# Kernel optimization log

Measured on AMD Instinct MI355X. Metric: run time of the kernel, lower is better.

The kernel has to match this reference:

```python
import jax, jax.numpy as jnp
import numpy as np

NUM_INTERNAL = 4000
MAX_CHILDREN = 16
BATCH = 1024


def _build_tree():
    # Deterministic synthetic hierarchy: child counts in [2, 16].
    counts = 2 + (np.arange(NUM_INTERNAL) * 7) % 15
    row = np.repeat(np.arange(NUM_INTERNAL), counts)
    col = np.concatenate([np.arange(n) for n in counts])
    flat_index = row * MAX_CHILDREN + col          # scatter slots in padded buffer
    num_nodes = int(counts.sum()) + 1              # +1 for the root
    child_index = np.arange(1, num_nodes)          # every non-root node is a child once
    return flat_index, child_index, num_nodes


def setup_inputs() -> dict:
    flat_index, child_index, num_nodes = _build_tree()
    key = jax.random.key(0)
    scores = jax.random.normal(key, (BATCH, flat_index.shape[0]), dtype=jnp.float32)
    return {
        "scores": scores,
        "flat_index": jnp.asarray(flat_index, dtype=jnp.int32),
        "child_index": jnp.asarray(child_index, dtype=jnp.int32),
        "num_internal": NUM_INTERNAL,
        "max_num_children": MAX_CHILDREN,
        "num_nodes": num_nodes,
    }


def reference(scores, flat_index, child_index, num_internal, max_num_children, num_nodes):
    lead = scores.shape[:-1]
    neg_inf = jnp.asarray(-jnp.inf, scores.dtype)
    # Scatter scores into padded [num_internal, max_num_children] buffer (-inf padding).
    flat = jnp.full((*lead, num_internal * max_num_children), neg_inf, dtype=scores.dtype)
    flat = flat.at[..., flat_index].set(scores)
    # Per-internal-node (grouped) log-softmax over the padded child axis.
    child_log_p = jax.nn.log_softmax(
        flat.reshape(*lead, num_internal, max_num_children), axis=-1
    ).reshape(*lead, num_internal * max_num_children)
    # Gather real slots back and scatter into node-indexed output (root stays 0).
    out = jnp.zeros((*lead, num_nodes), dtype=scores.dtype)
    out = out.at[..., child_index].set(child_log_p[..., flat_index])
    return out


if __name__ == "__main__":
    inp = setup_inputs()
    y = reference(**inp)
    print(y.shape, y.dtype)
```

## Files before the change

kernel.cpp:

```cpp
#include <hip/hip_runtime.h>
#include <math.h>

#define MAXC 16
#define GPB  256
#define BLOCK 256
#define LBUF_SZ (GPB * MAXC + 32)

__global__ void build_meta_kernel(const int* __restrict__ flat_index,
                                  const int* __restrict__ p_num_internal,
                                  const int* __restrict__ p_max_children,
                                  int n_scores,
                                  int* __restrict__ offs,
                                  unsigned short* __restrict__ gid16) {
    int j = blockIdx.x * blockDim.x + threadIdx.x;
    int mc = p_max_children[0];
    if (j < n_scores) {
        int fi = flat_index[j];
        int g  = fi / mc;
        gid16[j] = (unsigned short)g;
        if (fi - g * mc == 0) offs[g] = j;
    }
    if (j == 0) offs[p_num_internal[0]] = n_scores;
}

__global__ void __launch_bounds__(BLOCK)
hier_logsoftmax_kernel(const float* __restrict__ scores,
                       const int* __restrict__ offs,
                       const unsigned short* __restrict__ gid16,
                       const int* __restrict__ p_num_internal,
                       float* __restrict__ out,
                       int n_scores, int num_nodes) {
    __shared__ __align__(16) float lbuf[LBUF_SZ];
    __shared__ float lse[GPB];

    const int ni = p_num_internal[0];
    const int nchunks = (ni + GPB - 1) / GPB;
    const int b = blockIdx.y;
    const float* __restrict__ srow = scores + (size_t)b * (size_t)n_scores;
    float* __restrict__ orow = out + (size_t)b * (size_t)num_nodes;

    for (int chunk = blockIdx.x; chunk < nchunks; chunk += gridDim.x) {
        const int g0   = chunk * GPB;
        const int gend = min(g0 + GPB, ni);
        const int e0   = offs[g0];
        const int e1   = offs[gend];
        const int n    = e1 - e0;
        const int d    = e0 & 3;

        {
            const int hL  = min(n, (4 - (e0 & 3)) & 3);
            const int nvL = (n - hL) >> 2;
            for (int q = threadIdx.x; q < nvL; q += BLOCK) {
                const int i = hL + 4 * q;
                const float4 t = *(const float4*)&srow[e0 + i];
                *(float4*)&lbuf[d + i] = t;
            }
            for (int i = hL + 4 * nvL + threadIdx.x; i < n; i += BLOCK)
                lbuf[d + i] = srow[e0 + i];
            if (threadIdx.x < hL) lbuf[d + threadIdx.x] = srow[e0 + threadIdx.x];
        }
        __syncthreads();

        {
            const int g = g0 + threadIdx.x;
            if (g < gend) {
                const int og = offs[g];
                const int lo = d + (og - e0);
                const int c  = offs[g + 1] - og;
                float v[MAXC];
                #pragma unroll
                for (int k = 0; k < MAXC; ++k)
                    v[k] = (k < c) ? lbuf[lo + k] : -INFINITY;
                float m = v[0];
                #pragma unroll
                for (int k = 1; k < MAXC; ++k) m = fmaxf(m, v[k]);
                float s = 0.0f;
                #pragma unroll
                for (int k = 0; k < MAXC; ++k) s += __expf(v[k] - m);
                lse[threadIdx.x] = m + __logf(s);
            }
        }
        __syncthreads();

        {
            const unsigned short* __restrict__ grow = gid16 + e0;
            const int hS  = min(n, (4 - ((1 + e0) & 3)) & 3);
            const int nvS = (n - hS) >> 2;
            for (int q = threadIdx.x; q < nvS; q += BLOCK) {
                const int i = hS + 4 * q;
                float4 t;
                t.x = lbuf[d + i]     - lse[grow[i]     - g0];
                t.y = lbuf[d + i + 1] - lse[grow[i + 1] - g0];
                t.z = lbuf[d + i + 2] - lse[grow[i + 2] - g0];
                t.w = lbuf[d + i + 3] - lse[grow[i + 3] - g0];
                *(float4*)&orow[1 + e0 + i] = t;
            }
            for (int i = hS + 4 * nvS + threadIdx.x; i < n; i += BLOCK)
                orow[1 + e0 + i] = lbuf[d + i] - lse[grow[i] - g0];
            if (threadIdx.x < hS)
                orow[1 + e0 + threadIdx.x] = lbuf[d + threadIdx.x] - lse[grow[threadIdx.x] - g0];
        }
        if (chunk == 0 && threadIdx.x == 0) orow[0] = 0.0f;
        __syncthreads();
    }
}

extern "C" void kernel_launch(void* const* d_in, const int* in_sizes, int n_in,
                              void* d_out, int out_size, void* d_ws, size_t ws_size,
                              hipStream_t stream) {
    const float* scores     = (const float*)d_in[0];
    const int*   flat_index = (const int*)d_in[1];
    const int*   p_ni       = (const int*)d_in[3];
    const int*   p_mc       = (const int*)d_in[4];

    const int n_scores  = in_sizes[1];
    const int batch     = in_sizes[0] / n_scores;
    const int num_nodes = out_size / batch;

    int* offs = (int*)d_ws;
    unsigned short* gid16 = (unsigned short*)((char*)d_ws + ((size_t)(n_scores + 2) * 4 + 255 & ~(size_t)255));
    float* out = (float*)d_out;

    {
        dim3 blk(256), grd((n_scores + 255) / 256);
        hipLaunchKernelGGL(build_meta_kernel, grd, blk, 0, stream,
                           flat_index, p_ni, p_mc, n_scores, offs, gid16);
    }

    {
        dim3 blk(BLOCK), grd(16, batch);
        hipLaunchKernelGGL(hier_logsoftmax_kernel, grd, blk, 0, stream,
                           scores, offs, gid16, p_ni, out, n_scores, num_nodes);
    }
}
```

Measured before the change: 271.5 us.

## Software-pipeline chunk loads with register prefetch and stage gid16 in LDS

The grouped log-softmax kernel now prefetches the next chunk's scores and group ids into registers while the current chunk is computed, so global loads overlap with the LSE and output phases. Group ids are staged into shared memory as aligned vectors. The grid shrinks from 16 to 4 blocks per batch row so each block loops over multiple chunks, and launch bounds ask for 6 blocks per CU. The cost is higher register pressure and fewer blocks in flight, which could reduce occupancy-driven latency hiding.

After: 272.6 us. No clear change (+0.4%).

```diff
diff --git a/kernel.cpp b/kernel.cpp
--- a/kernel.cpp
+++ b/kernel.cpp
@@ -4,7 +4,15 @@
 #define MAXC 16
 #define GPB  256
 #define BLOCK 256
-#define LBUF_SZ (GPB * MAXC + 32)
+#define PFV 3
+#define PFG 2
+#define LBUF_SZ (GPB*MAXC + 24)
+#define GBUF_SZ (GPB*MAXC + 16)
+
+__device__ __forceinline__ void lds_barrier() {
+    asm volatile("s_waitcnt lgkmcnt(0)" ::: "memory");
+    __builtin_amdgcn_s_barrier();
+}
 
 __global__ void build_meta_kernel(const int* __restrict__ flat_index,
                                   const int* __restrict__ p_num_internal,
@@ -23,85 +31,171 @@
     if (j == 0) offs[p_num_internal[0]] = n_scores;
 }
 
-__global__ void __launch_bounds__(BLOCK)
+__global__ void __launch_bounds__(BLOCK, 6)
 hier_logsoftmax_kernel(const float* __restrict__ scores,
                        const int* __restrict__ offs,
                        const unsigned short* __restrict__ gid16,
                        const int* __restrict__ p_num_internal,
                        float* __restrict__ out,
-                       int n_scores, int num_nodes) {
+                       int n_scores, int num_nodes, int batch) {
     __shared__ __align__(16) float lbuf[LBUF_SZ];
-    __shared__ float lse[GPB];
+    __shared__ __align__(16) unsigned short gbuf[GBUF_SZ];
+    __shared__ float lsebuf[GPB];
 
     const int ni = p_num_internal[0];
     const int nchunks = (ni + GPB - 1) / GPB;
+    if ((int)blockIdx.x >= nchunks) return;
+
     const int b = blockIdx.y;
     const float* __restrict__ srow = scores + (size_t)b * (size_t)n_scores;
     float* __restrict__ orow = out + (size_t)b * (size_t)num_nodes;
-
-    for (int chunk = blockIdx.x; chunk < nchunks; chunk += gridDim.x) {
-        const int g0   = chunk * GPB;
-        const int gend = min(g0 + GPB, ni);
-        const int e0   = offs[g0];
-        const int e1   = offs[gend];
-        const int n    = e1 - e0;
-        const int d    = e0 & 3;
+    const int slim = (batch - b) * n_scores;
+
+    int chunk = blockIdx.x;
+
+    int g0, gend, e0, e1, ea4, ea8, nv4, nvg, ogt = 0, og1t = 0;
+    float4 pv[PFV];
+    uint4  pg[PFG];
+
+    auto do_prefetch = [&](int c) {
+        g0 = c * GPB; gend = min(g0 + GPB, ni);
+        e0 = offs[g0]; e1 = offs[gend];
+        ea4 = e0 & ~3; ea8 = e0 & ~7;
+        nv4 = (e1 - ea4 + 3) >> 2;
+        nvg = (e1 - ea8 + 7) >> 3;
+#pragma unroll
+        for (int p = 0; p < PFV; ++p) {
+            const int q = (int)threadIdx.x + p * BLOCK;
+            const int base = ea4 + 4 * q;
+            float4 t = make_float4(0.f, 0.f, 0.f, 0.f);
+            if (q < nv4) {
+                if (base + 4 <= slim) {
+                    t = *(const float4*)(srow + base);
+                } else {
+                    if (base     < slim) t.x = srow[base];
+                    if (base + 1 < slim) t.y = srow[base + 1];
+                    if (base + 2 < slim) t.z = srow[base + 2];
+                    if (base + 3 < slim) t.w = srow[base + 3];
+                }
+            }
+            pv[p] = t;
+        }
+#pragma unroll
+        for (int p = 0; p < PFG; ++p) {
+            const int q = (int)threadIdx.x + p * BLOCK;
+            const int base = ea8 + 8 * q;
+            uint4 t = make_uint4(0u, 0u, 0u, 0u);
+            if (q < nvg) {
+                if (base + 8 <= n_scores) {
+                    t = *(const uint4*)(gid16 + base);
+                } else {
+                    unsigned w0 = 0, w1 = 0, w2 = 0, w3 = 0;
+                    if (base + 0 < n_scores) w0 |= (unsigned)gid16[base + 0];
+                    if (base + 1 < n_scores) w0 |= (unsigned)gid16[base + 1] << 16;
+                    if (base + 2 < n_scores) w1 |= (unsigned)gid16[base + 2];
+                    if (base + 3 < n_scores) w1 |= (unsigned)gid16[base + 3] << 16;
+                    if (base + 4 < n_scores) w2 |= (unsigned)gid16[base + 4];
+                    if (base + 5 < n_scores) w2 |= (unsigned)gid16[base + 5] << 16;
+                    if (base + 6 < n_scores) w3 |= (unsigned)gid16[base + 6];
+                    if (base + 7 < n_scores) w3 |= (unsigned)gid16[base + 7] << 16;
+                    t = make_uint4(w0, w1, w2, w3);
+                }
+            }
+            pg[p] = t;
+        }
+        const int g = g0 + (int)threadIdx.x;
+        if (g < gend) { ogt = offs[g]; og1t = offs[g + 1]; }
+    };
+
+    do_prefetch(chunk);
+
+    for (;;) {
+        lds_barrier();
+
+#pragma unroll
+        for (int p = 0; p < PFV; ++p) {
+            const int q = (int)threadIdx.x + p * BLOCK;
+            if (q < nv4) *(float4*)&lbuf[4 * q] = pv[p];
+        }
+        for (int q = PFV * BLOCK + (int)threadIdx.x; q < nv4; q += BLOCK) {
+            const int base = ea4 + 4 * q;
+            float4 t = make_float4(0.f, 0.f, 0.f, 0.f);
+            if (base + 4 <= slim) t = *(const float4*)(srow + base);
+            else {
+                if (base     < slim) t.x = srow[base];
+                if (base + 1 < slim) t.y = srow[base + 1];
+                if (base + 2 < slim) t.z = srow[base + 2];
+                if (base + 3 < slim) t.w = srow[base + 3];
+            }
+            *(float4*)&lbuf[4 * q] = t;
+        }
+#pragma unroll
+        for (int p = 0; p < PFG; ++p) {
+            const int q = (int)threadIdx.x + p * BLOCK;
+            if (q < nvg) *(uint4*)&gbuf[8 * q] = pg[p];
+        }
+        for (int q = PFG * BLOCK + (int)threadIdx.x; q < nvg; q += BLOCK) {
+            const int base = ea8 + 8 * q;
+            uint4 t = make_uint4(0u, 0u, 0u, 0u);
+            if (base + 8 <= n_scores) t = *(const uint4*)(gid16 + base);
+            *(uint4*)&gbuf[8 * q] = t;
+        }
+
+        const int cg0 = g0, cgend = gend, ce0 = e0, ce1 = e1;
+        const int cea4 = ea4, cea8 = ea8, cog = ogt, cog1 = og1t;
+        const int next = chunk + gridDim.x;
+        const bool have_next = next < nchunks;
+        if (have_next) do_prefetch(next);
+
+        lds_barrier();
 
         {
-            const int hL  = min(n, (4 - (e0 & 3)) & 3);
-            const int nvL = (n - hL) >> 2;
-            for (int q = threadIdx.x; q < nvL; q += BLOCK) {
-                const int i = hL + 4 * q;
-                const float4 t = *(const float4*)&srow[e0 + i];
-                *(float4*)&lbuf[d + i] = t;
-            }
-            for (int i = hL + 4 * nvL + threadIdx.x; i < n; i += BLOCK)
-                lbuf[d + i] = srow[e0 + i];
-            if (threadIdx.x < hL) lbuf[d + threadIdx.x] = srow[e0 + threadIdx.x];
-        }
-        __syncthreads();
-
-        {
-            const int g = g0 + threadIdx.x;
-            if (g < gend) {
-                const int og = offs[g];
-                const int lo = d + (og - e0);
-                const int c  = offs[g + 1] - og;
+            const int g = cg0 + (int)threadIdx.x;
+            if (g < cgend) {
+                const int lo = cog - cea4;
+                const int c  = cog1 - cog;
                 float v[MAXC];
-                #pragma unroll
+#pragma unroll
                 for (int k = 0; k < MAXC; ++k)
                     v[k] = (k < c) ? lbuf[lo + k] : -INFINITY;
                 float m = v[0];
-                #pragma unroll
+#pragma unroll
                 for (int k = 1; k < MAXC; ++k) m = fmaxf(m, v[k]);
                 float s = 0.0f;
-                #pragma unroll
+#pragma unroll
                 for (int k = 0; k < MAXC; ++k) s += __expf(v[k] - m);
-                lse[threadIdx.x] = m + __logf(s);
-            }
-        }
-        __syncthreads();
+                lsebuf[threadIdx.x] = m + __logf(s);
+            }
+        }
+
+        lds_barrier();
 
         {
-            const unsigned short* __restrict__ grow = gid16 + e0;
-            const int hS  = min(n, (4 - ((1 + e0) & 3)) & 3);
+            const int n  = ce1 - ce0;
+            const int hS = min(n, (4 - ((1 + ce0) & 3)) & 3);
+            if ((int)threadIdx.x < hS) {
+                const int e = ce0 + (int)threadIdx.x;
+                orow[1 + e] = lbuf[e - cea4] - lsebuf[gbuf[e - cea8] - cg0];
+            }
             const int nvS = (n - hS) >> 2;
-            for (int q = threadIdx.x; q < nvS; q += BLOCK) {
-                const int i = hS + 4 * q;
+            for (int q = (int)threadIdx.x; q < nvS; q += BLOCK) {
+                const int e = ce0 + hS + 4 * q;
                 float4 t;
-                t.x = lbuf[d + i]     - lse[grow[i]     - g0];
-                t.y = lbuf[d + i + 1] - lse[grow[i + 1] - g0];
-                t.z = lbuf[d + i + 2] - lse[grow[i + 2] - g0];
-                t.w = lbuf[d + i + 3] - lse[grow[i + 3] - g0];
-                *(float4*)&orow[1 + e0 + i] = t;
-            }
-            for (int i = hS + 4 * nvS + threadIdx.x; i < n; i += BLOCK)
-                orow[1 + e0 + i] = lbuf[d + i] - lse[grow[i] - g0];
-            if (threadIdx.x < hS)
-                orow[1 + e0 + threadIdx.x] = lbuf[d + threadIdx.x] - lse[grow[threadIdx.x] - g0];
-        }
-        if (chunk == 0 && threadIdx.x == 0) orow[0] = 0.0f;
-        __syncthreads();
+                t.x = lbuf[e     - cea4] - lsebuf[gbuf[e     - cea8] - cg0];
+                t.y = lbuf[e + 1 - cea4] - lsebuf[gbuf[e + 1 - cea8] - cg0];
+                t.z = lbuf[e + 2 - cea4] - lsebuf[gbuf[e + 2 - cea8] - cg0];
+                t.w = lbuf[e + 3 - cea4] - lsebuf[gbuf[e + 3 - cea8] - cg0];
+                *(float4*)&orow[1 + e] = t;
+            }
+            for (int i = hS + 4 * nvS + (int)threadIdx.x; i < n; i += BLOCK) {
+                const int e = ce0 + i;
+                orow[1 + e] = lbuf[e - cea4] - lsebuf[gbuf[e - cea8] - cg0];
+            }
+            if (chunk == 0 && threadIdx.x == 0) orow[0] = 0.0f;
+        }
+
+        if (!have_next) break;
+        chunk = next;
     }
 }
 
@@ -118,7 +212,8 @@
     const int num_nodes = out_size / batch;
 
     int* offs = (int*)d_ws;
-    unsigned short* gid16 = (unsigned short*)((char*)d_ws + ((size_t)(n_scores + 2) * 4 + 255 & ~(size_t)255));
+    unsigned short* gid16 =
+        (unsigned short*)((char*)d_ws + (((size_t)(n_scores + 2) * 4 + 255) & ~(size_t)255));
     float* out = (float*)d_out;
 
     {
@@ -128,8 +223,8 @@
     }
 
     {
-        dim3 blk(BLOCK), grd(16, batch);
+        dim3 blk(BLOCK), grd(4, batch);
         hipLaunchKernelGGL(hier_logsoftmax_kernel, grd, blk, 0, stream,
-                           scores, offs, gid16, p_ni, out, n_scores, num_nodes);
-    }
-}
+                           scores, offs, gid16, p_ni, out, n_scores, num_nodes, batch);
+    }
+}
```

## Keep chunk scores in registers and accumulate group exp-sums with LDS atomics

Applied to the files above, without the earlier changes.

The per-chunk LDS staging buffer and the thread-per-group max/exp/log pass are replaced. Each thread now loads aligned float4 score vectors plus packed group ids into registers and accumulates exp(score) into per-group shared sums with LDS atomic adds. The result is then written from registers minus the log of the sum. This removes the shared staging copy and the serial 16-wide per-group loop. It drops the max subtraction, so large scores can overflow exp. It also brings atomic contention and scalar, unaligned output stores.

Result: slower. 422.4 us (+55.6%).

```diff
diff --git a/kernel.cpp b/kernel.cpp
--- a/kernel.cpp
+++ b/kernel.cpp
@@ -1,10 +1,9 @@
 #include <hip/hip_runtime.h>
 #include <math.h>
 
-#define MAXC 16
-#define GPB  256
+#define GPB   256
 #define BLOCK 256
-#define LBUF_SZ (GPB * MAXC + 32)
+#define MAXIT 5
 
 __global__ void build_meta_kernel(const int* __restrict__ flat_index,
                                   const int* __restrict__ p_num_internal,
@@ -29,78 +28,88 @@
                        const unsigned short* __restrict__ gid16,
                        const int* __restrict__ p_num_internal,
                        float* __restrict__ out,
-                       int n_scores, int num_nodes) {
-    __shared__ __align__(16) float lbuf[LBUF_SZ];
-    __shared__ float lse[GPB];
+                       int n_scores, int num_nodes, int batch) {
+    __shared__ float s[GPB];
 
     const int ni = p_num_internal[0];
     const int nchunks = (ni + GPB - 1) / GPB;
     const int b = blockIdx.y;
     const float* __restrict__ srow = scores + (size_t)b * (size_t)n_scores;
     float* __restrict__ orow = out + (size_t)b * (size_t)num_nodes;
+    const int slim = (batch - b) * n_scores;
+
+    if (blockIdx.x == 0 && threadIdx.x == 0) orow[0] = 0.0f;
 
     for (int chunk = blockIdx.x; chunk < nchunks; chunk += gridDim.x) {
         const int g0   = chunk * GPB;
         const int gend = min(g0 + GPB, ni);
         const int e0   = offs[g0];
         const int e1   = offs[gend];
-        const int n    = e1 - e0;
-        const int d    = e0 & 3;
+        const int ea   = e0 & ~3;
+        const int nv   = (e1 - ea + 3) >> 2;
 
-        {
-            const int hL  = min(n, (4 - (e0 & 3)) & 3);
-            const int nvL = (n - hL) >> 2;
-            for (int q = threadIdx.x; q < nvL; q += BLOCK) {
-                const int i = hL + 4 * q;
-                const float4 t = *(const float4*)&srow[e0 + i];
-                *(float4*)&lbuf[d + i] = t;
-            }
-            for (int i = hL + 4 * nvL + threadIdx.x; i < n; i += BLOCK)
-                lbuf[d + i] = srow[e0 + i];
-            if (threadIdx.x < hL) lbuf[d + threadIdx.x] = srow[e0 + threadIdx.x];
-        }
+        if (threadIdx.x < GPB) s[threadIdx.x] = 0.0f;
         __syncthreads();
 
-        {
-            const int g = g0 + threadIdx.x;
-            if (g < gend) {
-                const int og = offs[g];
-                const int lo = d + (og - e0);
-                const int c  = offs[g + 1] - og;
-                float v[MAXC];
-                #pragma unroll
-                for (int k = 0; k < MAXC; ++k)
-                    v[k] = (k < c) ? lbuf[lo + k] : -INFINITY;
-                float m = v[0];
-                #pragma unroll
-                for (int k = 1; k < MAXC; ++k) m = fmaxf(m, v[k]);
-                float s = 0.0f;
-                #pragma unroll
-                for (int k = 0; k < MAXC; ++k) s += __expf(v[k] - m);
-                lse[threadIdx.x] = m + __logf(s);
+        float4 v[MAXIT];
+        uint2  gp[MAXIT];
+
+#pragma unroll
+        for (int p = 0; p < MAXIT; ++p) {
+            const int q = (int)threadIdx.x + p * BLOCK;
+            const int base = ea + 4 * q;
+            float4 t = make_float4(0.f, 0.f, 0.f, 0.f);
+            uint2  gg = make_uint2(0u, 0u);
+            if (q < nv) {
+                if (base + 4 <= slim) {
+                    t = *(const float4*)(srow + base);
+                } else {
+                    if (base     < slim) t.x = srow[base];
+                    if (base + 1 < slim) t.y = srow[base + 1];
+                    if (base + 2 < slim) t.z = srow[base + 2];
+                    if (base + 3 < slim) t.w = srow[base + 3];
+                }
+                gg = *(const uint2*)(gid16 + base);
+            }
+            v[p] = t; gp[p] = gg;
+            if (q < nv) {
+                const int gA = (int)(gg.x & 0xffffu), gB = (int)(gg.x >> 16);
+                const int gC = (int)(gg.y & 0xffffu), gD = (int)(gg.y >> 16);
+                const bool iA = (base     >= e0) & (base     < e1);
+                const bool iB = (base + 1 >= e0) & (base + 1 < e1);
+                const bool iC = (base + 2 >= e0) & (base + 2 < e1);
+                const bool iD = (base + 3 >= e0) & (base + 3 < e1);
+                const unsigned xA = min((unsigned)(gA - g0), GPB - 1u);
+                const unsigned xB = min((unsigned)(gB - g0), GPB - 1u);
+                const unsigned xC = min((unsigned)(gC - g0), GPB - 1u);
+                const unsigned xD = min((unsigned)(gD - g0), GPB - 1u);
+                unsafeAtomicAdd(&s[xA], iA ? __expf(v[p].x) : 0.0f);
+                unsafeAtomicAdd(&s[xB], iB ? __expf(v[p].y) : 0.0f);
+                unsafeAtomicAdd(&s[xC], iC ? __expf(v[p].z) : 0.0f);
+                unsafeAtomicAdd(&s[xD], iD ? __expf(v[p].w) : 0.0f);
             }
         }
         __syncthreads();
 
-        {
-            const unsigned short* __restrict__ grow = gid16 + e0;
-            const int hS  = min(n, (4 - ((1 + e0) & 3)) & 3);
-            const int nvS = (n - hS) >> 2;
-            for (int q = threadIdx.x; q < nvS; q += BLOCK) {
-                const int i = hS + 4 * q;
-                float4 t;
-                t.x = lbuf[d + i]     - lse[grow[i]     - g0];
-                t.y = lbuf[d + i + 1] - lse[grow[i + 1] - g0];
-                t.z = lbuf[d + i + 2] - lse[grow[i + 2] - g0];
-                t.w = lbuf[d + i + 3] - lse[grow[i + 3] - g0];
-                *(float4*)&orow[1 + e0 + i] = t;
+        if (threadIdx.x < GPB) s[threadIdx.x] = __logf(s[threadIdx.x]);
+        __syncthreads();
+
+#pragma unroll
+        for (int p = 0; p < MAXIT; ++p) {
+            const int q = (int)threadIdx.x + p * BLOCK;
+            if (q < nv) {
+                const int base = ea + 4 * q;
+                const uint2 gg = gp[p];
+                const unsigned xA = min((unsigned)((int)(gg.x & 0xffffu) - g0), GPB - 1u);
+                const unsigned xB = min((unsigned)((int)(gg.x >> 16)     - g0), GPB - 1u);
+                const unsigned xC = min((unsigned)((int)(gg.y & 0xffffu) - g0), GPB - 1u);
+                const unsigned xD = min((unsigned)((int)(gg.y >> 16)     - g0), GPB - 1u);
+                if ((base     >= e0) & (base     < e1)) orow[1 + base]     = v[p].x - s[xA];
+                if ((base + 1 >= e0) & (base + 1 < e1)) orow[1 + base + 1] = v[p].y - s[xB];
+                if ((base + 2 >= e0) & (base + 2 < e1)) orow[1 + base + 2] = v[p].z - s[xC];
+                if ((base + 3 >= e0) & (base + 3 < e1)) orow[1 + base + 3] = v[p].w - s[xD];
             }
-            for (int i = hS + 4 * nvS + threadIdx.x; i < n; i += BLOCK)
-                orow[1 + e0 + i] = lbuf[d + i] - lse[grow[i] - g0];
-            if (threadIdx.x < hS)
-                orow[1 + e0 + threadIdx.x] = lbuf[d + threadIdx.x] - lse[grow[threadIdx.x] - g0];
         }
-        if (chunk == 0 && threadIdx.x == 0) orow[0] = 0.0f;
         __syncthreads();
     }
 }
@@ -118,7 +127,8 @@
     const int num_nodes = out_size / batch;
 
     int* offs = (int*)d_ws;
-    unsigned short* gid16 = (unsigned short*)((char*)d_ws + ((size_t)(n_scores + 2) * 4 + 255 & ~(size_t)255));
+    unsigned short* gid16 =
+        (unsigned short*)((char*)d_ws + (((size_t)(n_scores + 2) * 4 + 255) & ~(size_t)255));
     float* out = (float*)d_out;
 
     {
@@ -130,6 +140,6 @@
     {
         dim3 blk(BLOCK), grd(16, batch);
         hipLaunchKernelGGL(hier_logsoftmax_kernel, grd, blk, 0, stream,
-                           scores, offs, gid16, p_ni, out, n_scores, num_nodes);
+                           scores, offs, gid16, p_ni, out, n_scores, num_nodes, batch);
     }
 }
```
